# Optimization experiments

Hardware: AMD Instinct MI355X
Metric: run time of the kernel (lower is better)

The kernel has to match this reference:

```python
import jax, jax.numpy as jnp
import numpy as np

N_NODES = 100000
N_REL = 8
IN_FEATS = 64
ATTN_FEATS = 32
NUM_HEADS = 4
N_EDGES = 800000
NEG_SLOPE = 0.2


def setup_inputs() -> dict:
    key = jax.random.key(0)
    ks = jax.random.split(key, 11)
    s = 0.05
    return {
        "feat": jax.random.normal(ks[0], (N_NODES, IN_FEATS), jnp.float32),
        "quality_emb": jax.random.normal(ks[1], (N_NODES, IN_FEATS), jnp.float32),
        "fc_src_w": jax.random.normal(ks[2], (N_REL, IN_FEATS, ATTN_FEATS * NUM_HEADS), jnp.float32) * s,
        "fc_src_b": jax.random.normal(ks[3], (N_REL, ATTN_FEATS * NUM_HEADS), jnp.float32) * s,
        "fc_qual_w": jax.random.normal(ks[4], (N_REL, IN_FEATS, ATTN_FEATS * NUM_HEADS), jnp.float32) * s,
        "fc_qual_b": jax.random.normal(ks[5], (N_REL, ATTN_FEATS * NUM_HEADS), jnp.float32) * s,
        "attn": jax.random.normal(ks[6], (N_REL, NUM_HEADS, ATTN_FEATS), jnp.float32) * s,
        "src": jax.random.randint(ks[7], (N_EDGES,), 0, N_NODES, jnp.int64),
        "dst": jax.random.randint(ks[8], (N_EDGES,), 0, N_NODES, jnp.int64),
        "r_type": jax.random.randint(ks[9], (N_EDGES,), 0, N_REL, jnp.int64),
        "nid": jax.random.randint(ks[10], (N_EDGES,), 0, N_NODES, jnp.int64),
    }


def reference(feat, quality_emb, fc_src_w, fc_src_b, fc_qual_w, fc_qual_b, attn,
              src, dst, r_type, nid):
    # gather_mm(feat[src], fc_src_w, idx_b=r_type) == project per node for all
    # relations (grouped GEMM), then gather [src, r_type] per edge.
    feat_proj = jnp.einsum('ni,rio->nro', feat, fc_src_w)          # [N, R, H*D]
    el = feat_proj[src, r_type] + fc_src_b[r_type]                 # [E, H*D]

    qual_proj = jnp.einsum('ni,rio->nro', quality_emb, fc_qual_w)  # [N, R, H*D]
    qual = qual_proj[nid, r_type] + fc_qual_b[r_type]              # [E, H*D]

    e = jax.nn.leaky_relu((el + qual).reshape(-1, NUM_HEADS, ATTN_FEATS), NEG_SLOPE)
    score = jnp.sum(e * attn[r_type], axis=-1)                     # [E, H]

    # edge softmax grouped by destination node, per head
    m = jax.ops.segment_max(score, dst, num_segments=N_NODES)      # [N, H]
    p = jnp.exp(score - m[dst])
    denom = jax.ops.segment_sum(p, dst, num_segments=N_NODES)      # [N, H]
    a = p / denom[dst]                                             # [E, H]

    # narre: messages use raw source features, weighted by attention
    msg = feat[src][:, None, :] * a[:, :, None]                    # [E, H, IN]
    ft = jax.ops.segment_sum(msg, dst, num_segments=N_NODES)       # [N, H, IN]
    return ft
```

## Files before the change

### kernel.cpp

```cpp
#include <hip/hip_runtime.h>
#include <hip/hip_bf16.h>

#define RELS 8
#define HDD 128
#define NH 4
#define STILES 4

typedef __attribute__((ext_vector_type(8))) short bf16x8;
typedef __attribute__((ext_vector_type(4))) float f32x4;
typedef unsigned short u16;

__device__ __forceinline__ u16 f2b(float v){
  union { float f; unsigned u; } x; x.f = v;
  unsigned r = x.u + 0x7fffu + ((x.u >> 16) & 1u);
  return (u16)(r >> 16);
}
__device__ __forceinline__ float b2f(u16 h){
  union { unsigned u; float f; } x; x.u = ((unsigned)h) << 16; return x.f;
}

template<int CTRL>
__device__ __forceinline__ float dpp_mov(float x){
  union { float f; int i; } u; u.f = x;
  u.i = __builtin_amdgcn_update_dpp(0, u.i, CTRL, 0xF, 0xF, false);
  return u.f;
}
__device__ __forceinline__ float row_sum16(float v){
  v += dpp_mov<0x121>(v);
  v += dpp_mov<0x122>(v);
  v += dpp_mov<0x124>(v);
  v += dpp_mov<0x128>(v);
  return v;
}

__global__ void k_combo(const float* __restrict__ wsrc, const float* __restrict__ wqual,
                        const float* __restrict__ bsrc, const float* __restrict__ bqual,
                        u16* __restrict__ Wt, float* __restrict__ biasc,
                        const float* __restrict__ feat, const float* __restrict__ qual,
                        u16* __restrict__ featb, u16* __restrict__ qualb, int total,
                        const int* __restrict__ dst, const int* __restrict__ rt,
                        int* __restrict__ deg, int* __restrict__ rankD,
                        int* __restrict__ rcnt, int E,
                        int B0, int B2){
  int b = blockIdx.x, t = threadIdx.x;
  if (b < B2){
    __shared__ int lh[RELS];
    if (t < RELS) lh[t] = 0;
    __syncthreads();
    int e = b*256 + t;
    if (e < E){
      rankD[e] = atomicAdd(&deg[dst[e]], 1);
      atomicAdd(&lh[rt[e]], 1);
    }
    __syncthreads();
    if (t < RELS && lh[t]) atomicAdd(&rcnt[t], lh[t]);
  } else if (b < B2 + B0){
    int g = (b - B2)*256 + t;
    if (g < RELS*HDD*HDD){
      int r = g >> 14, rem = g & 16383, n = rem >> 7, k = rem & 127;
      float v = (k < 64) ? wsrc[r*8192 + k*128 + n] : wqual[r*8192 + (k-64)*128 + n];
      Wt[g] = f2b(v);
    } else {
      int bb = g - RELS*HDD*HDD;
      if (bb < RELS*HDD) biasc[bb] = bsrc[bb] + bqual[bb];
    }
  } else {
    int g = ((b - B2 - B0)*256 + t) * 8;
    const float* sp; u16* dp;
    if (g < total){ sp = feat; dp = featb; }
    else { g -= total; if (g >= total) return; sp = qual; dp = qualb; }
    float4 a = *(const float4*)(sp + g);
    float4 c = *(const float4*)(sp + g + 4);
    union { u16 h[8]; uint4 v; } o;
    o.h[0]=f2b(a.x); o.h[1]=f2b(a.y); o.h[2]=f2b(a.z); o.h[3]=f2b(a.w);
    o.h[4]=f2b(c.x); o.h[5]=f2b(c.y); o.h[6]=f2b(c.z); o.h[7]=f2b(c.w);
    *(uint4*)(dp + g) = o.v;
  }
}

__global__ void k_scan_a(const int* __restrict__ deg, int* __restrict__ offD,
                         int* __restrict__ bsums, int N){
  __shared__ int s[256];
  int t = threadIdx.x, i = blockIdx.x*256 + t;
  int v = (i < N) ? deg[i] : 0;
  s[t] = v; __syncthreads();
  for (int off=1; off<256; off<<=1){
    int x = (t >= off) ? s[t-off] : 0;
    __syncthreads();
    s[t] += x;
    __syncthreads();
  }
  if (i < N) offD[i] = s[t] - v;
  if (t == 255) bsums[blockIdx.x] = s[255];
}

__global__ void k_scan_b(const int* __restrict__ bsums, int* __restrict__ bsums_sc,
                         int* __restrict__ offD, const int* __restrict__ rcnt,
                         int* __restrict__ roff, int* __restrict__ rcur,
                         int NBLK, int N){
  __shared__ int s[512];
  int t = threadIdx.x;
  int v = (t < NBLK) ? bsums[t] : 0;
  s[t] = v; __syncthreads();
  for (int off=1; off<512; off<<=1){
    int x = (t >= off) ? s[t-off] : 0;
    __syncthreads();
    s[t] += x;
    __syncthreads();
  }
  if (t < NBLK) bsums_sc[t] = s[t] - v;
  if (t == NBLK-1) offD[N] = s[t];
  if (t == 0){
    int a = 0;
    for (int r=0;r<RELS;r++){ roff[r]=a; rcur[r]=a; a += rcnt[r]; }
    roff[RELS] = a;
  }
}

__global__ void k_scan_c(int* __restrict__ offD, const int* __restrict__ bsums_sc, int N){
  int i = blockIdx.x*256 + threadIdx.x;
  if (i < N) offD[i] += bsums_sc[i >> 8];
}

__global__ void k_scatter(const int* __restrict__ dst, const int* __restrict__ rt,
                          const int* __restrict__ src, const int* __restrict__ nid,
                          const int* __restrict__ offD, const int* __restrict__ rankD,
                          int* __restrict__ rcur,
                          int* __restrict__ srcD, int* __restrict__ srcR,
                          int* __restrict__ nidR, int* __restrict__ posR, int E){
  __shared__ int lh[RELS], lb[RELS];
  int t = threadIdx.x;
  if (t < RELS) lh[t] = 0;
  __syncthreads();
  int e = blockIdx.x*256 + t;
  int r = 0, rank = 0, pd = 0, sv = 0;
  if (e < E){
    int d = dst[e];
    sv = src[e];
    pd = offD[d] + rankD[e];
    srcD[pd] = sv;
    r = rt[e];
    rank = atomicAdd(&lh[r], 1);
  }
  __syncthreads();
  if (t < RELS && lh[t] > 0) lb[t] = atomicAdd(&rcur[t], lh[t]);
  __syncthreads();
  if (e < E){
    int pr = lb[r] + rank;
    srcR[pr] = sv;
    nidR[pr] = nid[e];
    posR[pr] = pd;
  }
}

__global__ __launch_bounds__(256) void k_score(
    const u16* __restrict__ featb, const u16* __restrict__ qualb,
    const u16* __restrict__ Wt, const float* __restrict__ biasc,
    const float* __restrict__ attn,
    const int* __restrict__ srcR, const int* __restrict__ nidR,
    const int* __restrict__ posR, const int* __restrict__ roff,
    float* __restrict__ scoreD){
  __shared__ u16 As[2][64*128];
  __shared__ int pos_s[2][64];
  int t = threadIdx.x;

  int bid = blockIdx.x;
  int r = -1, base = 0, cntR = 0;
  {
    int acc0 = 0;
    int prev = roff[0];
    #pragma unroll
    for (int rr=0; rr<RELS; rr++){
      int nxt = roff[rr+1];
      int c = nxt - prev;
      int nb = (c + STILES*64 - 1) / (STILES*64);
      if (r < 0 && bid < acc0 + nb){
        int ch = bid - acc0;
        r = rr; base = prev + ch*STILES*64; cntR = min(STILES*64, c - ch*STILES*64);
      }
      acc0 += nb;
      prev = nxt;
    }
  }
  if (r < 0) return;
  int Tact = (cntR + 63) >> 6;

  int mloc = t >> 2, part = t & 3;
  int lane = t & 63, w = t >> 6;
  int lr = lane & 15, lq = lane >> 4;

  const u16* wbase = Wt + r*16384 + (w*32)*128;
  bf16x8 wfrag[2][4];
  #pragma unroll
  for (int mt=0; mt<2; mt++)
    #pragma unroll
    for (int kt=0; kt<4; kt++)
      wfrag[mt][kt] = *(const bf16x8*)(wbase + (mt*16 + lr)*128 + kt*32 + lq*8);

  float attn_p[2][4], attn_n[2][4];
  f32x4 biasv[2];
  #pragma unroll
  for (int mt=0; mt<2; mt++)
    #pragma unroll
    for (int i=0; i<4; i++){
      int c = w*32 + mt*16 + lq*4 + i;
      float a = attn[r*128 + c];
      biasv[mt][i] = biasc[r*128 + c];
      attn_p[mt][i] = a;
      attn_n[mt][i] = 0.2f*a;
    }

  const u16* basep = (part < 2) ? featb : qualb;
  int halfoff = (part & 1)*32;
  int myidx[STILES], mypos[STILES];
  #pragma unroll
  for (int tt=0; tt<STILES; tt++){
    int eloc = tt*64 + mloc;
    bool v = (eloc < cntR);
    int gi = base + eloc;
    myidx[tt] = v ? ((part < 2) ? srcR[gi] : nidR[gi]) : -1;
    mypos[tt] = v ? posR[gi] : -1;
  }

  uint4 pre[2][4];
  auto fetch = [&](int pb, int idxval){
    if (idxval >= 0){
      const uint4* pv = (const uint4*)(basep + (long long)idxval*64 + halfoff);
      pre[pb][0]=pv[0]; pre[pb][1]=pv[1]; pre[pb][2]=pv[2]; pre[pb][3]=pv[3];
    } else {
      uint4 z = {0,0,0,0};
      pre[pb][0]=z; pre[pb][1]=z; pre[pb][2]=z; pre[pb][3]=z;
    }
  };

  fetch(0, myidx[0]);
  fetch(1, myidx[1]);
  #pragma unroll
  for (int tt=0; tt<STILES; tt++){
    if (tt >= Tact) break;
    const int p = tt & 1;
    uint4* As_v = (uint4*)As[p];
    #pragma unroll
    for (int i=0;i<4;i++){
      int c = part*4 + i;
      As_v[mloc*16 + (c ^ part ^ (mloc & 7))] = pre[p][i];
    }
    if (part == 0) pos_s[p][mloc] = mypos[tt];
    if (tt+2 < STILES) fetch(p, myidx[tt+2]);
    __syncthreads();

    f32x4 acc[4][2];
    #pragma unroll
    for (int et=0; et<4; et++){ acc[et][0]=biasv[0]; acc[et][1]=biasv[1]; }
    #pragma unroll
    for (int et=0; et<4; et++){
      #pragma unroll
      for (int kt=0; kt<4; kt++){
        bf16x8 bf = *(const bf16x8*)&As[p][(et*16 + lr)*128 + (((kt*4 + lq) ^ kt ^ (lr & 7))*8)];
        acc[et][0] = __builtin_amdgcn_mfma_f32_16x16x32_bf16(wfrag[0][kt], bf, acc[et][0], 0, 0, 0);
        acc[et][1] = __builtin_amdgcn_mfma_f32_16x16x32_bf16(wfrag[1][kt], bf, acc[et][1], 0, 0, 0);
      }
    }

    float s0v=0.f, s1v=0.f, s2v=0.f, s3v=0.f;
    #pragma unroll
    for (int mt=0; mt<2; mt++)
      #pragma unroll
      for (int i=0; i<4; i++){
        float x0 = acc[0][mt][i];
        s0v = __builtin_fmaf(fmaxf(x0,0.f), attn_p[mt][i], s0v);
        s0v = __builtin_fmaf(fminf(x0,0.f), attn_n[mt][i], s0v);
        float x1 = acc[1][mt][i];
        s1v = __builtin_fmaf(fmaxf(x1,0.f), attn_p[mt][i], s1v);
        s1v = __builtin_fmaf(fminf(x1,0.f), attn_n[mt][i], s1v);
        float x2 = acc[2][mt][i];
        s2v = __builtin_fmaf(fmaxf(x2,0.f), attn_p[mt][i], s2v);
        s2v = __builtin_fmaf(fminf(x2,0.f), attn_n[mt][i], s2v);
        float x3 = acc[3][mt][i];
        s3v = __builtin_fmaf(fmaxf(x3,0.f), attn_p[mt][i], s3v);
        s3v = __builtin_fmaf(fminf(x3,0.f), attn_n[mt][i], s3v);
      }
    s0v += __shfl_xor(s0v, 16); s0v += __shfl_xor(s0v, 32);
    s1v += __shfl_xor(s1v, 16); s1v += __shfl_xor(s1v, 32);
    s2v += __shfl_xor(s2v, 16); s2v += __shfl_xor(s2v, 32);
    s3v += __shfl_xor(s3v, 16); s3v += __shfl_xor(s3v, 32);
    float v01 = (lq & 1) ? s1v : s0v;
    float v23 = (lq & 1) ? s3v : s2v;
    float v = (lq & 2) ? v23 : v01;
    v = __expf(v);
    int pd = pos_s[p][lane];
    if (pd >= 0) scoreD[(long long)pd*4 + w] = v;
  }
}

__global__ __launch_bounds__(256) void k_agg(
    const int* __restrict__ offD, const int* __restrict__ srcD,
    const float* __restrict__ scoreD,
    const u16* __restrict__ featb, float* __restrict__ out, int N){
  __shared__ float ps[4][64][4];
  __shared__ int   ss[4][64];
  int wv = threadIdx.x >> 6, lane = threadIdx.x & 63;
  int node = blockIdx.x*4 + wv;
  if (node >= N) return;
  int s0 = offD[node], s1 = offD[node+1];
  int deg = s1 - s0;
  float a0=0.f, a1=0.f, a2=0.f, a3=0.f;
  if (deg > 0){
    float d0=0.f,d1=0.f,d2=0.f,d3=0.f;
    for (int c=0; c<deg; c+=64){
      int j = c + lane;
      float p0=0.f,p1=0.f,p2=0.f,p3=0.f; int sv=0;
      if (j < deg){
        float4 sc = *(const float4*)&scoreD[(long long)(s0+j)*4];
        sv = srcD[s0+j];
        p0=sc.x; p1=sc.y; p2=sc.z; p3=sc.w;
      }
      d0+=p0; d1+=p1; d2+=p2; d3+=p3;
      float4 pv = { p0, p1, p2, p3 };
      *(float4*)&ps[wv][lane][0] = pv;
      ss[wv][lane] = sv;
      __builtin_amdgcn_wave_barrier();
      int cnt = min(64, deg - c);
      #pragma unroll 4
      for (int e=0; e<cnt; e++){
        float4 pe = *(const float4*)&ps[wv][e][0];
        float fv = b2f(featb[(long long)ss[wv][e]*64 + lane]);
        a0 += pe.x*fv; a1 += pe.y*fv; a2 += pe.z*fv; a3 += pe.w*fv;
      }
      __builtin_amdgcn_wave_barrier();
    }
    d0=row_sum16(d0); d1=row_sum16(d1); d2=row_sum16(d2); d3=row_sum16(d3);
    #pragma unroll
    for (int off=16; off<64; off<<=1){
      d0+=__shfl_xor(d0,off); d1+=__shfl_xor(d1,off);
      d2+=__shfl_xor(d2,off); d3+=__shfl_xor(d3,off);
    }
    a0 *= 1.f/d0; a1 *= 1.f/d1; a2 *= 1.f/d2; a3 *= 1.f/d3;
  }
  float* op = out + (long long)node*256;
  op[lane]       = a0;
  op[64 + lane]  = a1;
  op[128 + lane] = a2;
  op[192 + lane] = a3;
}

extern "C" void kernel_launch(void* const* d_in, const int* in_sizes, int n_in,
                              void* d_out, int out_size, void* d_ws, size_t ws_size,
                              hipStream_t stream) {
  const float* feat  = (const float*)d_in[0];
  const float* qual  = (const float*)d_in[1];
  const float* wsrc  = (const float*)d_in[2];
  const float* bsrc  = (const float*)d_in[3];
  const float* wqual = (const float*)d_in[4];
  const float* bqual = (const float*)d_in[5];
  const float* attn  = (const float*)d_in[6];
  const int* src = (const int*)d_in[7];
  const int* dst = (const int*)d_in[8];
  const int* rt  = (const int*)d_in[9];
  const int* nid = (const int*)d_in[10];
  const int E = in_sizes[7];
  const int N = in_sizes[0] / 64;
  float* out = (float*)d_out;

  char* p = (char*)d_ws;
  auto alloc = [&](size_t bytes) -> void* {
    void* q = (void*)p;
    p += (bytes + 255) & ~(size_t)255;
    return q;
  };
  float* scoreD  = (float*)alloc((size_t)E*4*4);
  u16*  featb    = (u16*)  alloc((size_t)N*64*2);
  u16*  qualb    = (u16*)  alloc((size_t)N*64*2);
  u16*  Wt       = (u16*)  alloc((size_t)RELS*HDD*HDD*2);
  float* biasc   = (float*)alloc((size_t)RELS*HDD*4);
  int*  srcD     = (int*)  alloc((size_t)E*4);
  int*  srcR     = (int*)  alloc((size_t)E*4);
  int*  nidR     = (int*)  alloc((size_t)E*4);
  int*  posR     = (int*)  alloc((size_t)E*4);
  int*  rankD    = (int*)  alloc((size_t)E*4);
  int*  offD     = (int*)  alloc((size_t)(N+1)*4);
  int*  bsums    = (int*)  alloc(4096);
  int*  bsums_sc = (int*)  alloc(4096);
  char* zbase = p;
  int*  deg      = (int*)  alloc((size_t)N*4);
  int*  rcnt     = (int*)  alloc(32);
  int*  roff     = (int*)  alloc(64);
  int*  rcur     = (int*)  alloc(32);
  size_t zbytes = (size_t)(p - zbase);

  hipMemsetAsync(zbase, 0, zbytes, stream);

  int total = N*64;
  int totw = RELS*HDD*HDD + RELS*HDD;
  int B0 = (totw + 255)/256;
  int B1 = ((2*total)/8 + 255)/256;
  int B2 = (E + 255)/256;
  k_combo<<<B0+B1+B2, 256, 0, stream>>>(wsrc, wqual, bsrc, bqual, Wt, biasc,
                                        feat, qual, featb, qualb, total,
                                        dst, rt, deg, rankD, rcnt, E, B0, B2);
  int NBLK = (N + 255)/256;
  k_scan_a<<<NBLK, 256, 0, stream>>>(deg, offD, bsums, N);
  k_scan_b<<<1, 512, 0, stream>>>(bsums, bsums_sc, offD, rcnt, roff, rcur, NBLK, N);
  k_scan_c<<<NBLK, 256, 0, stream>>>(offD, bsums_sc, N);
  k_scatter<<<B2, 256, 0, stream>>>(dst, rt, src, nid, offD, rankD, rcur, srcD, srcR, nidR, posR, E);
  int NBS = (E + STILES*64 - 1)/(STILES*64) + RELS;
  k_score<<<NBS, 256, 0, stream>>>(featb, qualb, Wt, biasc, attn, srcR, nidR, posR, roff, scoreD);
  k_agg<<<(N + 3)/4, 256, 0, stream>>>(offD, srcD, scoreD, featb, out, N);
}
```

Before: 352.3 us.

## Overlap dst-degree atomics with score GEMM using an extra helper wave

Moves the per-destination degree counting out of the preprocessing kernel and into a fifth wave of the score kernel, so the scattered atomics run alongside the MFMA work. The helper wave matches the compute waves' barrier count. Scores are written in relation order, and a new permutation kernel moves them and the source ids into dst-CSR order after the scan. The relation-sort scatter now runs before the scan and derives offsets from the counts directly. This adds an extra pass over the scores and a score buffer, and depends on the barrier counts staying matched.

```diff
diff --git a/kernel.cpp b/kernel.cpp
--- a/kernel.cpp
+++ b/kernel.cpp
@@ -38,24 +38,20 @@
                         u16* __restrict__ Wt, float* __restrict__ biasc,
                         const float* __restrict__ feat, const float* __restrict__ qual,
                         u16* __restrict__ featb, u16* __restrict__ qualb, int total,
-                        const int* __restrict__ dst, const int* __restrict__ rt,
-                        int* __restrict__ deg, int* __restrict__ rankD,
+                        const int* __restrict__ rt,
                         int* __restrict__ rcnt, int E,
-                        int B0, int B2){
+                        int BH, int B0){
   int b = blockIdx.x, t = threadIdx.x;
-  if (b < B2){
+  if (b < BH){
     __shared__ int lh[RELS];
     if (t < RELS) lh[t] = 0;
     __syncthreads();
-    int e = b*256 + t;
-    if (e < E){
-      rankD[e] = atomicAdd(&deg[dst[e]], 1);
+    for (int e = b*256 + t; e < E; e += BH*256)
       atomicAdd(&lh[rt[e]], 1);
-    }
     __syncthreads();
     if (t < RELS && lh[t]) atomicAdd(&rcnt[t], lh[t]);
-  } else if (b < B2 + B0){
-    int g = (b - B2)*256 + t;
+  } else if (b < BH + B0){
+    int g = (b - BH)*256 + t;
     if (g < RELS*HDD*HDD){
       int r = g >> 14, rem = g & 16383, n = rem >> 7, k = rem & 127;
       float v = (k < 64) ? wsrc[r*8192 + k*128 + n] : wqual[r*8192 + (k-64)*128 + n];
@@ -65,7 +61,7 @@
       if (bb < RELS*HDD) biasc[bb] = bsrc[bb] + bqual[bb];
     }
   } else {
-    int g = ((b - B2 - B0)*256 + t) * 8;
+    int g = ((b - BH - B0)*256 + t) * 8;
     const float* sp; u16* dp;
     if (g < total){ sp = feat; dp = featb; }
     else { g -= total; if (g >= total) return; sp = qual; dp = qualb; }
@@ -78,6 +74,39 @@
   }
 }
 
+__global__ void k_scatter(const int* __restrict__ rt,
+                          const int* __restrict__ src, const int* __restrict__ nid,
+                          const int* __restrict__ dst,
+                          const int* __restrict__ rcnt, int* __restrict__ rcur,
+                          int* __restrict__ srcR, int* __restrict__ nidR,
+                          int* __restrict__ dstR, int E){
+  __shared__ int lh[RELS], lb[RELS];
+  int t = threadIdx.x;
+  if (t < RELS) lh[t] = 0;
+  __syncthreads();
+  int e = blockIdx.x*256 + t;
+  int r = 0, rank = 0, sv = 0, nv = 0, dv = 0;
+  if (e < E){
+    sv = src[e]; nv = nid[e]; dv = dst[e];
+    r = rt[e];
+    rank = atomicAdd(&lh[r], 1);
+  }
+  __syncthreads();
+  if (t < RELS){
+    int ro = 0;
+    #pragma unroll
+    for (int i=0;i<RELS;i++) if (i < t) ro += rcnt[i];
+    if (lh[t] > 0) lb[t] = ro + atomicAdd(&rcur[t], lh[t]);
+  }
+  __syncthreads();
+  if (e < E){
+    int pr = lb[r] + rank;
+    srcR[pr] = sv;
+    nidR[pr] = nv;
+    dstR[pr] = dv;
+  }
+}
+
 __global__ void k_scan_a(const int* __restrict__ deg, int* __restrict__ offD,
                          int* __restrict__ bsums, int N){
   __shared__ int s[256];
@@ -95,9 +124,7 @@
 }
 
 __global__ void k_scan_b(const int* __restrict__ bsums, int* __restrict__ bsums_sc,
-                         int* __restrict__ offD, const int* __restrict__ rcnt,
-                         int* __restrict__ roff, int* __restrict__ rcur,
-                         int NBLK, int N){
+                         int* __restrict__ offD, int NBLK, int N){
   __shared__ int s[512];
   int t = threadIdx.x;
   int v = (t < NBLK) ? bsums[t] : 0;
@@ -110,11 +137,6 @@
   }
   if (t < NBLK) bsums_sc[t] = s[t] - v;
   if (t == NBLK-1) offD[N] = s[t];
-  if (t == 0){
-    int a = 0;
-    for (int r=0;r<RELS;r++){ roff[r]=a; rcur[r]=a; a += rcnt[r]; }
-    roff[RELS] = a;
-  }
 }
 
 __global__ void k_scan_c(int* __restrict__ offD, const int* __restrict__ bsums_sc, int N){
@@ -122,68 +144,52 @@
   if (i < N) offD[i] += bsums_sc[i >> 8];
 }
 
-__global__ void k_scatter(const int* __restrict__ dst, const int* __restrict__ rt,
-                          const int* __restrict__ src, const int* __restrict__ nid,
-                          const int* __restrict__ offD, const int* __restrict__ rankD,
-                          int* __restrict__ rcur,
-                          int* __restrict__ srcD, int* __restrict__ srcR,
-                          int* __restrict__ nidR, int* __restrict__ posR, int E){
-  __shared__ int lh[RELS], lb[RELS];
-  int t = threadIdx.x;
-  if (t < RELS) lh[t] = 0;
-  __syncthreads();
-  int e = blockIdx.x*256 + t;
-  int r = 0, rank = 0, pd = 0, sv = 0;
-  if (e < E){
-    int d = dst[e];
-    sv = src[e];
-    pd = offD[d] + rankD[e];
-    srcD[pd] = sv;
-    r = rt[e];
-    rank = atomicAdd(&lh[r], 1);
-  }
-  __syncthreads();
-  if (t < RELS && lh[t] > 0) lb[t] = atomicAdd(&rcur[t], lh[t]);
-  __syncthreads();
-  if (e < E){
-    int pr = lb[r] + rank;
-    srcR[pr] = sv;
-    nidR[pr] = nid[e];
-    posR[pr] = pd;
-  }
-}
-
-__global__ __launch_bounds__(256) void k_score(
+__global__ __launch_bounds__(320) void k_score(
     const u16* __restrict__ featb, const u16* __restrict__ qualb,
     const u16* __restrict__ Wt, const float* __restrict__ biasc,
     const float* __restrict__ attn,
     const int* __restrict__ srcR, const int* __restrict__ nidR,
-    const int* __restrict__ posR, const int* __restrict__ roff,
-    float* __restrict__ scoreD){
+    const int* __restrict__ dstR, const int* __restrict__ rcnt,
+    int* __restrict__ deg, int* __restrict__ rankR,
+    float* __restrict__ scoreR, int E){
   __shared__ u16 As[2][64*128];
-  __shared__ int pos_s[2][64];
   int t = threadIdx.x;
 
   int bid = blockIdx.x;
   int r = -1, base = 0, cntR = 0;
   {
-    int acc0 = 0;
-    int prev = roff[0];
+    int acc0 = 0, st = 0;
     #pragma unroll
     for (int rr=0; rr<RELS; rr++){
-      int nxt = roff[rr+1];
-      int c = nxt - prev;
-      int nb = (c + STILES*64 - 1) / (STILES*64);
+      int c = rcnt[rr];
+      int nb = (c + 255) >> 8;
       if (r < 0 && bid < acc0 + nb){
         int ch = bid - acc0;
-        r = rr; base = prev + ch*STILES*64; cntR = min(STILES*64, c - ch*STILES*64);
+        r = rr; base = st + ch*256; cntR = min(256, c - ch*256);
       }
       acc0 += nb;
-      prev = nxt;
+      st += c;
     }
   }
   if (r < 0) return;
   int Tact = (cntR + 63) >> 6;
+
+  if (t >= 256){
+    int hl = t - 256;
+    int eh0=-1,eh1=-1,eh2=-1,eh3=-1;
+    int rk0=0,rk1=0,rk2=0,rk3=0;
+    if (hl < cntR)     { eh0 = base+hl;     rk0 = atomicAdd(&deg[dstR[eh0]],1); }
+    if (64+hl < cntR)  { eh1 = base+64+hl;  rk1 = atomicAdd(&deg[dstR[eh1]],1); }
+    if (128+hl < cntR) { eh2 = base+128+hl; rk2 = atomicAdd(&deg[dstR[eh2]],1); }
+    if (192+hl < cntR) { eh3 = base+192+hl; rk3 = atomicAdd(&deg[dstR[eh3]],1); }
+    for (int i=0;i<Tact;i++)
+      __builtin_amdgcn_s_barrier();
+    if (eh0>=0) rankR[eh0]=rk0;
+    if (eh1>=0) rankR[eh1]=rk1;
+    if (eh2>=0) rankR[eh2]=rk2;
+    if (eh3>=0) rankR[eh3]=rk3;
+    return;
+  }
 
   int mloc = t >> 2, part = t & 3;
   int lane = t & 63, w = t >> 6;
@@ -212,14 +218,12 @@
 
   const u16* basep = (part < 2) ? featb : qualb;
   int halfoff = (part & 1)*32;
-  int myidx[STILES], mypos[STILES];
+  int myidx[STILES];
   #pragma unroll
   for (int tt=0; tt<STILES; tt++){
     int eloc = tt*64 + mloc;
-    bool v = (eloc < cntR);
     int gi = base + eloc;
-    myidx[tt] = v ? ((part < 2) ? srcR[gi] : nidR[gi]) : -1;
-    mypos[tt] = v ? posR[gi] : -1;
+    myidx[tt] = (eloc < cntR) ? ((part < 2) ? srcR[gi] : nidR[gi]) : -1;
   }
 
   uint4 pre[2][4];
@@ -245,9 +249,9 @@
       int c = part*4 + i;
       As_v[mloc*16 + (c ^ part ^ (mloc & 7))] = pre[p][i];
     }
-    if (part == 0) pos_s[p][mloc] = mypos[tt];
     if (tt+2 < STILES) fetch(p, myidx[tt+2]);
-    __syncthreads();
+    asm volatile("s_waitcnt lgkmcnt(0)" ::: "memory");
+    __builtin_amdgcn_s_barrier();
 
     f32x4 acc[4][2];
     #pragma unroll
@@ -288,9 +292,26 @@
     float v23 = (lq & 1) ? s3v : s2v;
     float v = (lq & 2) ? v23 : v01;
     v = __expf(v);
-    int pd = pos_s[p][lane];
-    if (pd >= 0) scoreD[(long long)pd*4 + w] = v;
-  }
+    int eout = tt*64 + lane;
+    if (eout < cntR) scoreR[(size_t)w*E + base + eout] = v;
+  }
+}
+
+__global__ void k_perm(const int* __restrict__ dstR, const int* __restrict__ rankR,
+                       const int* __restrict__ srcR, const float* __restrict__ scoreR,
+                       const int* __restrict__ offD,
+                       float* __restrict__ scoreD, int* __restrict__ srcD, int E){
+  int pr = blockIdx.x*256 + threadIdx.x;
+  if (pr >= E) return;
+  int d = dstR[pr];
+  int pd = offD[d] + rankR[pr];
+  float4 sc;
+  sc.x = scoreR[pr];
+  sc.y = scoreR[(size_t)E + pr];
+  sc.z = scoreR[(size_t)2*E + pr];
+  sc.w = scoreR[(size_t)3*E + pr];
+  *(float4*)&scoreD[(long long)pd*4] = sc;
+  srcD[pd] = srcR[pr];
 }
 
 __global__ __launch_bounds__(256) void k_agg(
@@ -369,6 +390,7 @@
     return q;
   };
   float* scoreD  = (float*)alloc((size_t)E*4*4);
+  float* scoreR  = (float*)alloc((size_t)E*4*4);
   u16*  featb    = (u16*)  alloc((size_t)N*64*2);
   u16*  qualb    = (u16*)  alloc((size_t)N*64*2);
   u16*  Wt       = (u16*)  alloc((size_t)RELS*HDD*HDD*2);
@@ -376,15 +398,14 @@
   int*  srcD     = (int*)  alloc((size_t)E*4);
   int*  srcR     = (int*)  alloc((size_t)E*4);
   int*  nidR     = (int*)  alloc((size_t)E*4);
-  int*  posR     = (int*)  alloc((size_t)E*4);
-  int*  rankD    = (int*)  alloc((size_t)E*4);
+  int*  dstR     = (int*)  alloc((size_t)E*4);
+  int*  rankR    = (int*)  alloc((size_t)E*4);
   int*  offD     = (int*)  alloc((size_t)(N+1)*4);
   int*  bsums    = (int*)  alloc(4096);
   int*  bsums_sc = (int*)  alloc(4096);
   char* zbase = p;
   int*  deg      = (int*)  alloc((size_t)N*4);
   int*  rcnt     = (int*)  alloc(32);
-  int*  roff     = (int*)  alloc(64);
   int*  rcur     = (int*)  alloc(32);
   size_t zbytes = (size_t)(p - zbase);
 
@@ -392,18 +413,22 @@
 
   int total = N*64;
   int totw = RELS*HDD*HDD + RELS*HDD;
+  int BH = 512;
   int B0 = (totw + 255)/256;
   int B1 = ((2*total)/8 + 255)/256;
   int B2 = (E + 255)/256;
-  k_combo<<<B0+B1+B2, 256, 0, stream>>>(wsrc, wqual, bsrc, bqual, Wt, biasc,
+  k_combo<<<BH+B0+B1, 256, 0, stream>>>(wsrc, wqual, bsrc, bqual, Wt, biasc,
                                         feat, qual, featb, qualb, total,
-                                        dst, rt, deg, rankD, rcnt, E, B0, B2);
+                                        rt, rcnt, E, BH, B0);
+  k_scatter<<<B2, 256, 0, stream>>>(rt, src, nid, dst, rcnt, rcur,
+                                    srcR, nidR, dstR, E);
+  int NBS = B2 + RELS;
+  k_score<<<NBS, 320, 0, stream>>>(featb, qualb, Wt, biasc, attn,
+                                   srcR, nidR, dstR, rcnt, deg, rankR, scoreR, E);
   int NBLK = (N + 255)/256;
   k_scan_a<<<NBLK, 256, 0, stream>>>(deg, offD, bsums, N);
-  k_scan_b<<<1, 512, 0, stream>>>(bsums, bsums_sc, offD, rcnt, roff, rcur, NBLK, N);
+  k_scan_b<<<1, 512, 0, stream>>>(bsums, bsums_sc, offD, NBLK, N);
   k_scan_c<<<NBLK, 256, 0, stream>>>(offD, bsums_sc, N);
-  k_scatter<<<B2, 256, 0, stream>>>(dst, rt, src, nid, offD, rankD, rcur, srcD, srcR, nidR, posR, E);
-  int NBS = (E + STILES*64 - 1)/(STILES*64) + RELS;
-  k_score<<<NBS, 256, 0, stream>>>(featb, qualb, Wt, biasc, attn, srcR, nidR, posR, roff, scoreD);
+  k_perm<<<B2, 256, 0, stream>>>(dstR, rankR, srcR, scoreR, offD, scoreD, srcD, E);
   k_agg<<<(N + 3)/4, 256, 0, stream>>>(offD, srcD, scoreD, featb, out, N);
 }
```

Measured after the change: 370.1 us. +5.1%, slower.
